# Optimization experiments

Measured on AMD Instinct MI355X. Metric: run time of the kernel, lower is better.

Reference implementation:

```python
import jax, jax.numpy as jnp
import numpy as np

K_HOPS = 3
ALPHA = 0.3
DELTA = 0.5
KL_EPS = 1e-10
BN_EPS = 1e-5
DEG_MIN = 1e-6

B, T, N, F_IN, H, T_OUT = 8, 12, 1536, 1, 64, 12
HID2 = 2 * H  # MLP hidden width = 128


def setup_inputs() -> dict:
    key = jax.random.key(0)
    ks = jax.random.split(key, 20)
    s = 0.05
    TH = T * H
    inp = {
        "x": jax.random.normal(ks[0], (B, T, N, F_IN), jnp.float32),
        # AdaptiveBiDiffConv weights (stored as (in, out))
        "W1": jax.random.normal(ks[1], (F_IN, H), jnp.float32) * s,
        "W2": jax.random.normal(ks[2], (F_IN, H), jnp.float32) * s,
        # encoder MLPBlock: Linear(TH,128) ReLU Linear(128,128) ReLU Linear(128,64) + proj(TH,64), BN(64)
        "enc_w1": jax.random.normal(ks[3], (TH, HID2), jnp.float32) * s,
        "enc_b1": jnp.zeros((HID2,), jnp.float32),
        "enc_w2": jax.random.normal(ks[4], (HID2, HID2), jnp.float32) * s,
        "enc_b2": jnp.zeros((HID2,), jnp.float32),
        "enc_w3": jax.random.normal(ks[5], (HID2, H), jnp.float32) * s,
        "enc_b3": jnp.zeros((H,), jnp.float32),
        "enc_proj": jax.random.normal(ks[6], (TH, H), jnp.float32) * s,
        "enc_bn_g": jnp.ones((H,), jnp.float32),
        "enc_bn_b": jnp.zeros((H,), jnp.float32),
        "enc_bn_m": jnp.zeros((H,), jnp.float32),
        "enc_bn_v": jnp.ones((H,), jnp.float32),
        # decoder MLPBlock: Linear(64,128) ReLU Linear(128,128) ReLU Linear(128,12) + proj(64,12), BN(12)
        "dec_w1": jax.random.normal(ks[7], (H, HID2), jnp.float32) * s,
        "dec_b1": jnp.zeros((HID2,), jnp.float32),
        "dec_w2": jax.random.normal(ks[8], (HID2, HID2), jnp.float32) * s,
        "dec_b2": jnp.zeros((HID2,), jnp.float32),
        "dec_w3": jax.random.normal(ks[9], (HID2, T_OUT), jnp.float32) * s,
        "dec_b3": jnp.zeros((T_OUT,), jnp.float32),
        "dec_proj": jax.random.normal(ks[10], (H, T_OUT), jnp.float32) * s,
        "dec_bn_g": jnp.ones((T_OUT,), jnp.float32),
        "dec_bn_b": jnp.zeros((T_OUT,), jnp.float32),
        "dec_bn_m": jnp.zeros((T_OUT,), jnp.float32),
        "dec_bn_v": jnp.ones((T_OUT,), jnp.float32),
    }
    return inp


def _row_norm(A):
    return A / jnp.maximum(A.sum(-1, keepdims=True), DEG_MIN)


def _mlp_block(z, w1, b1, w2, b2, w3, b3, proj, g, be, m, v):
    h = jax.nn.relu(z @ w1 + b1)
    h = jax.nn.relu(h @ w2 + b2)
    o = (h @ w3 + b3) + z @ proj
    # BatchNorm1d, eval mode over last (channel) axis
    return (o - m) / jnp.sqrt(v + BN_EPS) * g + be


def _forward(x, W1, W2,
             enc_w1, enc_b1, enc_w2, enc_b2, enc_w3, enc_b3, enc_proj,
             enc_bn_g, enc_bn_b, enc_bn_m, enc_bn_v,
             dec_w1, dec_b1, dec_w2, dec_b2, dec_w3, dec_b3, dec_proj,
             dec_bn_g, dec_bn_b, dec_bn_m, dec_bn_v):
    b, t, n, _ = x.shape
    # ---- KL adjacency (fused form: avoids (B,N,N,T) broadcast) ----
    p = jax.nn.softmax(jnp.transpose(x[..., 0], (0, 2, 1)), axis=-1)  # (B,N,T)
    logp = jnp.log(p + KL_EPS)
    # kl[b,i,j] = sum_t p_i (logp_i - logp_j)
    kl = jnp.sum(p * logp, axis=-1, keepdims=True) - jnp.einsum('bit,bjt->bij', p, logp)
    A = (kl < DELTA).astype(x.dtype)  # (B,N,N)
    A_fwd = _row_norm(A)
    A_bwd = _row_norm(jnp.swapaxes(A, -1, -2))
    # ---- bidirectional diffusion conv (x_k never updated in original loop) ----
    x_flow = x[..., :1]                    # (B,T,N,1)
    x_res = x_flow @ W1                    # (B,T,N,H)
    xw = x_flow @ W2                       # (B,T,N,H)
    fwd = jnp.einsum('bij,btjh->btih', A_fwd, xw)
    bwd = jnp.einsum('bij,btjh->btih', A_bwd, xw)
    x_p = jax.nn.relu(x_res + K_HOPS * (ALPHA * fwd + (1.0 - ALPHA) * bwd))
    # ---- temporal MLP encoder/decoder ----
    x_flat = jnp.transpose(x_p, (0, 2, 1, 3)).reshape(b, n, t * x_p.shape[-1])  # (B,N,T*H)
    x_e = _mlp_block(x_flat, enc_w1, enc_b1, enc_w2, enc_b2, enc_w3, enc_b3,
                     enc_proj, enc_bn_g, enc_bn_b, enc_bn_m, enc_bn_v)  # (B,N,H)
    x_d = _mlp_block(x_e, dec_w1, dec_b1, dec_w2, dec_b2, dec_w3, dec_b3,
                     dec_proj, dec_bn_g, dec_bn_b, dec_bn_m, dec_bn_v)  # (B,N,T_out)
    return jnp.transpose(x_d, (0, 2, 1))[..., None]  # (B,T_out,N,1)


def reference(x, W1, W2,
              enc_w1, enc_b1, enc_w2, enc_b2, enc_w3, enc_b3, enc_proj,
              enc_bn_g, enc_bn_b, enc_bn_m, enc_bn_v,
              dec_w1, dec_b1, dec_w2, dec_b2, dec_w3, dec_b3, dec_proj,
              dec_bn_g, dec_bn_b, dec_bn_m, dec_bn_v):
    return _forward(x, W1, W2,
                    enc_w1, enc_b1, enc_w2, enc_b2, enc_w3, enc_b3, enc_proj,
                    enc_bn_g, enc_bn_b, enc_bn_m, enc_bn_v,
                    dec_w1, dec_b1, dec_w2, dec_b2, dec_w3, dec_b3, dec_proj,
                    dec_bn_g, dec_bn_b, dec_bn_m, dec_bn_v)
```

## Files before the change

### kernel.cpp

```cpp
#include <hip/hip_runtime.h>
#include <hip/hip_bf16.h>


namespace {

constexpr int Nn = 1536, TOUT = 12;

typedef __attribute__((ext_vector_type(8))) short bf8;
typedef __attribute__((ext_vector_type(4))) float f4;
typedef unsigned short ush;

__device__ __forceinline__ float b2f(__hip_bfloat16 v) { return __bfloat162float(v); }
__device__ __forceinline__ ush f2bu(float f) {
  union { __hip_bfloat16 h; ush u; } c; c.h = __float2bfloat16(f); return c.u;
}
__device__ __forceinline__ float bu2f(ush u) {
  union { unsigned int i; float f; } c; c.i = ((unsigned)u) << 16; return c.f;
}
__device__ __forceinline__ float ldraw(const void* p, size_t i, int fl) {
  return fl ? ((const float*)p)[i] : b2f(((const __hip_bfloat16*)p)[i]);
}

__device__ __forceinline__ int detect_fl(const void* x, int tid) {
  __shared__ int cnt;
  if (tid == 0) cnt = 0;
  __syncthreads();
  const ush* u = (const ush*)x;
  int c = 0;
#pragma unroll
  for (int s = 0; s < 16; ++s) {
    ush v = u[tid + s * 256];
    if (((v >> 7) & 0xFF) >= 140) c++;
  }
  atomicAdd(&cnt, c);
  __syncthreads();
  return (cnt > 64) ? 1 : 0;
}

struct SmallTab { const void* src[16]; int n[16]; int off[16]; };
struct RepTab { const void* src[8]; int Nc[8]; int NCT[8]; int lb[9]; };

__global__ __launch_bounds__(256) void prep_all(
    const void* __restrict__ xraw, SmallTab st, RepTab rt,
    int* __restrict__ flag, float* __restrict__ CS,
    float* __restrict__ xT, float* __restrict__ sd,
    ush* __restrict__ pA, ush* __restrict__ lA,
    ush* __restrict__ phi16, ush* __restrict__ plo16,
    ush* __restrict__ lhi16, ush* __restrict__ llo16,
    ush* __restrict__ Xc, ush* __restrict__ Wf) {
  int tid = threadIdx.x;
  int fl = detect_fl(xraw, tid);
  int blk = blockIdx.x;

  if (blk < 48) {
    int row = blk * 256 + tid;
    int b = row / Nn, n = row - b * Nn;
    float xv[12];
#pragma unroll
    for (int t = 0; t < 12; ++t)
      xv[t] = ldraw(xraw, (size_t)(b * 12 + t) * Nn + n, fl);
    float mx = xv[0];
#pragma unroll
    for (int t = 1; t < 12; ++t) mx = fmaxf(mx, xv[t]);
    float e[12], Z = 0.f;
#pragma unroll
    for (int t = 0; t < 12; ++t) { e[t] = expf(xv[t] - mx); Z += e[t]; }
    float invZ = 1.f / Z;
    float sacc = 0.f;
    ush pa[32], la[32], ph[16], pl[16], lh[16], ll[16];
#pragma unroll
    for (int k = 0; k < 32; ++k) { pa[k] = 0; la[k] = 0; }
#pragma unroll
    for (int k = 0; k < 16; ++k) { ph[k] = 0; pl[k] = 0; lh[k] = 0; ll[k] = 0; }
#pragma unroll
    for (int t = 0; t < 12; ++t) {
      float pv = e[t] * invZ;
      float lv = logf(pv + 1e-10f);
      sacc += pv * lv;
      xT[(size_t)row * 12 + t] = xv[t];
      ush phv = f2bu(pv);  float plv = pv - bu2f(phv);
      ush lhv = f2bu(lv);  float llv = lv - bu2f(lhv);
      pa[t] = phv; pa[16 + t] = f2bu(plv);
      la[t] = lhv; la[16 + t] = f2bu(llv);
      ph[t] = phv; pl[t] = f2bu(plv);
      lh[t] = lhv; ll[t] = f2bu(llv);
      Xc[((size_t)(b * 16 + t)) * Nn + n] = f2bu(xv[t]);
    }
    Xc[((size_t)(b * 16 + 12)) * Nn + n] = 0x3F80;
#pragma unroll
    for (int t = 13; t < 16; ++t) Xc[((size_t)(b * 16 + t)) * Nn + n] = 0;
    sd[row] = sacc;
    {
      uint4* d = (uint4*)(pA + (size_t)row * 32);
      const uint4* s = (const uint4*)pa;
      d[0] = s[0]; d[1] = s[1]; d[2] = s[2]; d[3] = s[3];
      uint4* d2 = (uint4*)(lA + (size_t)row * 32);
      const uint4* s2 = (const uint4*)la;
      d2[0] = s2[0]; d2[1] = s2[1]; d2[2] = s2[2]; d2[3] = s2[3];
      ((uint4*)(phi16 + (size_t)row * 16))[0] = ((const uint4*)ph)[0];
      ((uint4*)(phi16 + (size_t)row * 16))[1] = ((const uint4*)ph)[1];
      ((uint4*)(plo16 + (size_t)row * 16))[0] = ((const uint4*)pl)[0];
      ((uint4*)(plo16 + (size_t)row * 16))[1] = ((const uint4*)pl)[1];
      ((uint4*)(lhi16 + (size_t)row * 16))[0] = ((const uint4*)lh)[0];
      ((uint4*)(lhi16 + (size_t)row * 16))[1] = ((const uint4*)lh)[1];
      ((uint4*)(llo16 + (size_t)row * 16))[0] = ((const uint4*)ll)[0];
      ((uint4*)(llo16 + (size_t)row * 16))[1] = ((const uint4*)ll)[1];
    }
  } else if (blk < 146) {
    int idx = (blk - 48) * 256 + tid;
    if (idx >= rt.lb[8]) return;
    int mi = 0;
#pragma unroll
    for (int i = 1; i < 8; ++i) if (idx >= rt.lb[i]) mi = i;
    int li = idx - rt.lb[mi];
    int NCT = rt.NCT[mi], Nc = rt.Nc[mi];
    int per = NCT * 64;
    int c0 = li / per, rem = li - c0 * per;
    int ct = rem >> 6, l = rem & 63;
    int q = l >> 4, m = l & 15;
    int col = ct * 16 + m;
    ush* d = Wf + (size_t)idx * 8;
#pragma unroll
    for (int j = 0; j < 8; ++j) {
      int k = c0 * 32 + q * 8 + j;
      d[j] = (col < Nc) ? f2bu(ldraw(rt.src[mi], (size_t)k * Nc + col, fl)) : 0;
    }
  } else {
    for (int i = 0; i < 16; ++i)
      for (int e = tid; e < st.n[i]; e += 256)
        CS[st.off[i] + e] = ldraw(st.src[i], e, fl);
    if (tid == 0) flag[0] = fl;
  }
}

__global__ __launch_bounds__(256, 3) void klmlp(
    const float* __restrict__ xT,
    const ush* __restrict__ pA, const ush* __restrict__ lA,
    const ush* __restrict__ phi16, const ush* __restrict__ plo16,
    const ush* __restrict__ lhi16, const ush* __restrict__ llo16,
    const ush* __restrict__ Xc, const float* __restrict__ sd,
    const float* __restrict__ CS, const ush* __restrict__ Wf,
    const int* __restrict__ flag, void* __restrict__ outp) {
  __shared__ float xs[16][12], ccs[16][12];
  __shared__ float sfs[16][16], sbs[16][16];
  __shared__ float ws1[64], ws2[64];
  __shared__ ush hf[2048], hg[2048], xf[1024];
  __shared__ f4 red[4][64], red2[4][64];
  __shared__ union { ush T[2][4][512]; ush zf[12288]; } u;

  int tid = threadIdx.x, w = tid >> 6, l = tid & 63, q = l >> 4, n = l & 15;
  int bi = blockIdx.x;
  int r0 = bi * 16;
  int b = bi / 96;
  int rowb = b * Nn;

  if (tid < 192) {
    int rr = tid / 12, tt = tid - rr * 12;
    xs[rr][tt] = xT[(size_t)(r0 + rr) * 12 + tt];
  }

  {
    bf8 z8 = {0, 0, 0, 0, 0, 0, 0, 0};
    bf8 aP = *(const bf8*)(pA + ((size_t)(r0 + n)) * 32 + q * 8);
    bf8 aL = *(const bf8*)(lA + ((size_t)(r0 + n)) * 32 + q * 8);
    bf8 aPh = (q < 2) ? aP : z8;
    bf8 aLh = (q < 2) ? aL : z8;
    float selfI[4];
#pragma unroll
    for (int r = 0; r < 4; ++r) selfI[r] = sd[r0 + q * 4 + r];

    f4 accF = {0.f, 0.f, 0.f, 0.f}, accB = {0.f, 0.f, 0.f, 0.f};

    for (int jp = 0; jp < 12; ++jp) {
      int jl = w * 384 + jp * 32;
#pragma unroll
      for (int hh = 0; hh < 2; ++hh) {
        int jh = jl + hh * 16;
        size_t bb = ((size_t)(rowb + jh + n)) * 16 + (q & 1) * 8;
        bf8 bLh = *(const bf8*)(lhi16 + bb);
        bf8 bLo = *(const bf8*)(llo16 + bb);
        bf8 bPh = *(const bf8*)(phi16 + bb);
        bf8 bPo = *(const bf8*)(plo16 + bb);
        float selfJ = sd[rowb + jh + n];

        f4 s1 = {0.f, 0.f, 0.f, 0.f}, s2 = {0.f, 0.f, 0.f, 0.f};
        s1 = __builtin_amdgcn_mfma_f32_16x16x32_bf16(aP, bLh, s1, 0, 0, 0);
        s1 = __builtin_amdgcn_mfma_f32_16x16x32_bf16(aPh, bLo, s1, 0, 0, 0);
        s2 = __builtin_amdgcn_mfma_f32_16x16x32_bf16(aL, bPh, s2, 0, 0, 0);
        s2 = __builtin_amdgcn_mfma_f32_16x16x32_bf16(aLh, bPo, s2, 0, 0, 0);

        int qk = n >> 3, kj = n & 7;
#pragma unroll
        for (int r = 0; r < 4; ++r) {
          int pos = hh * 256 + (qk * 16 + q * 4 + r) * 8 + kj;
          u.T[0][w][pos] = (selfI[r] - s1[r] < 0.5f) ? (ush)0x3F80 : (ush)0;
          u.T[1][w][pos] = (selfJ - s2[r] < 0.5f) ? (ush)0x3F80 : (ush)0;
        }
      }
      bf8 af1 = *(const bf8*)(&u.T[0][w][(size_t)l * 8]);
      bf8 af2 = *(const bf8*)(&u.T[1][w][(size_t)l * 8]);
      bf8 xfr = *(const bf8*)(Xc + ((size_t)(b * 16 + n)) * Nn + jl + q * 8);
      accF = __builtin_amdgcn_mfma_f32_16x16x32_bf16(af1, xfr, accF, 0, 0, 0);
      accB = __builtin_amdgcn_mfma_f32_16x16x32_bf16(af2, xfr, accB, 0, 0, 0);
    }
    red[w][l] = accF;
    red2[w][l] = accB;
  }
  __syncthreads();

  if (w == 0) {
    f4 s = red[0][l] + red[1][l] + red[2][l] + red[3][l];
#pragma unroll
    for (int r = 0; r < 4; ++r) sfs[q * 4 + r][n] = s[r];
  } else if (w == 1) {
    f4 s = red2[0][l] + red2[1][l] + red2[2][l] + red2[3][l];
#pragma unroll
    for (int r = 0; r < 4; ++r) sbs[q * 4 + r][n] = s[r];
  } else if (w == 2) {
    ws1[l] = CS[l];
  } else {
    ws2[l] = CS[64 + l];
  }
  __syncthreads();
  if (tid < 192) {
    int rr = tid / 12, tt = tid - rr * 12;
    float irs = 1.f / fmaxf(sfs[rr][12], 1e-6f);
    float ics = 1.f / fmaxf(sbs[rr][12], 1e-6f);
    ccs[rr][tt] = 3.0f * (0.3f * sfs[rr][tt] * irs + 0.7f * sbs[rr][tt] * ics);
  }
  __syncthreads();

  auto zregen = [&](int c0) -> bf8 {
    int t = c0 >> 1, h0 = (c0 & 1) * 32 + q * 8;
    float xv = xs[n][t], cv = ccs[n][t];
    union { bf8 v; ush uu[8]; } au;
#pragma unroll
    for (int j = 0; j < 8; ++j)
      au.uu[j] = f2bu(fmaxf(fmaf(xv, ws1[h0 + j], cv * ws2[h0 + j]), 0.f));
    return au.v;
  };
  auto fpos = [&](int ct, int r) -> int {
    return ((ct >> 1) * 64 + ((ct & 1) * 2 + (n >> 3)) * 16 + q * 4 + r) * 8 + (n & 7);
  };

#pragma unroll
  for (int u6 = 0; u6 < 6; ++u6) {
    int c0 = w * 6 + u6;
    bf8 v = zregen(c0);
    *(bf8*)(&u.zf[((size_t)c0 * 64 + l) * 8]) = v;
  }
  __syncthreads();

  {
    f4 a0 = {0.f, 0.f, 0.f, 0.f}, a1 = {0.f, 0.f, 0.f, 0.f};
    for (int c0 = 0; c0 < 24; ++c0) {
      bf8 a = *(const bf8*)(&u.zf[((size_t)c0 * 64 + l) * 8]);
      const ush* wb = Wf + ((size_t)(c0 * 8 + 2 * w) * 64 + l) * 8;
      bf8 b0 = *(const bf8*)wb;
      bf8 b1 = *(const bf8*)(wb + 512);
      a0 = __builtin_amdgcn_mfma_f32_16x16x32_bf16(a, b0, a0, 0, 0, 0);
      a1 = __builtin_amdgcn_mfma_f32_16x16x32_bf16(a, b1, a1, 0, 0, 0);
    }
#pragma unroll
    for (int u2 = 0; u2 < 2; ++u2) {
      int ct = 2 * w + u2;
      f4 acc = u2 ? a1 : a0;
      float bz = CS[128 + ct * 16 + n];
#pragma unroll
      for (int r = 0; r < 4; ++r)
        hf[fpos(ct, r)] = f2bu(fmaxf(acc[r] + bz, 0.f));
    }
  }
  __syncthreads();

  {
    f4 a0 = {0.f, 0.f, 0.f, 0.f}, a1 = {0.f, 0.f, 0.f, 0.f};
    for (int c0 = 0; c0 < 4; ++c0) {
      bf8 a = *(const bf8*)(&hf[(size_t)(c0 * 64 + l) * 8]);
      const ush* wb = Wf + 98304 + ((size_t)(c0 * 8 + 2 * w) * 64 + l) * 8;
      bf8 b0 = *(const bf8*)wb;
      bf8 b1 = *(const bf8*)(wb + 512);
      a0 = __builtin_amdgcn_mfma_f32_16x16x32_bf16(a, b0, a0, 0, 0, 0);
      a1 = __builtin_amdgcn_mfma_f32_16x16x32_bf16(a, b1, a1, 0, 0, 0);
    }
    __syncthreads();
#pragma unroll
    for (int u2 = 0; u2 < 2; ++u2) {
      int ct = 2 * w + u2;
      f4 acc = u2 ? a1 : a0;
      float bz = CS[256 + ct * 16 + n];
#pragma unroll
      for (int r = 0; r < 4; ++r)
        hg[fpos(ct, r)] = f2bu(fmaxf(acc[r] + bz, 0.f));
    }
  }
  __syncthreads();

  {
    f4 a3 = {0.f, 0.f, 0.f, 0.f};
    for (int c0 = 0; c0 < 4; ++c0) {
      bf8 a = *(const bf8*)(&hg[(size_t)(c0 * 64 + l) * 8]);
      bf8 bb = *(const bf8*)(Wf + 114688 + ((size_t)(c0 * 4 + w) * 64 + l) * 8);
      a3 = __builtin_amdgcn_mfma_f32_16x16x32_bf16(a, bb, a3, 0, 0, 0);
    }
    for (int c0 = 0; c0 < 24; ++c0) {
      bf8 a = *(const bf8*)(&u.zf[((size_t)c0 * 64 + l) * 8]);
      bf8 bb = *(const bf8*)(Wf + 122880 + ((size_t)(c0 * 4 + w) * 64 + l) * 8);
      a3 = __builtin_amdgcn_mfma_f32_16x16x32_bf16(a, bb, a3, 0, 0, 0);
    }
    int col = w * 16 + n;
    float g = CS[448 + col], be = CS[512 + col], mm = CS[576 + col], vv = CS[640 + col];
    float sc = g / sqrtf(vv + 1e-5f);
    float sh = be - mm * sc;
    float bz = CS[384 + col];
#pragma unroll
    for (int r = 0; r < 4; ++r)
      xf[fpos(w, r)] = f2bu((a3[r] + bz) * sc + sh);
  }
  __syncthreads();

  {
    f4 a0 = {0.f, 0.f, 0.f, 0.f}, a1 = {0.f, 0.f, 0.f, 0.f};
    for (int c0 = 0; c0 < 2; ++c0) {
      bf8 a = *(const bf8*)(&xf[(size_t)(c0 * 64 + l) * 8]);
      const ush* wb = Wf + 172032 + ((size_t)(c0 * 8 + 2 * w) * 64 + l) * 8;
      bf8 b0 = *(const bf8*)wb;
      bf8 b1 = *(const bf8*)(wb + 512);
      a0 = __builtin_amdgcn_mfma_f32_16x16x32_bf16(a, b0, a0, 0, 0, 0);
      a1 = __builtin_amdgcn_mfma_f32_16x16x32_bf16(a, b1, a1, 0, 0, 0);
    }
    __syncthreads();
#pragma unroll
    for (int u2 = 0; u2 < 2; ++u2) {
      int ct = 2 * w + u2;
      f4 acc = u2 ? a1 : a0;
      float bz = CS[704 + ct * 16 + n];
#pragma unroll
      for (int r = 0; r < 4; ++r)
        hf[fpos(ct, r)] = f2bu(fmaxf(acc[r] + bz, 0.f));
    }
  }
  __syncthreads();

  {
    f4 a0 = {0.f, 0.f, 0.f, 0.f}, a1 = {0.f, 0.f, 0.f, 0.f};
    for (int c0 = 0; c0 < 4; ++c0) {
      bf8 a = *(const bf8*)(&hf[(size_t)(c0 * 64 + l) * 8]);
      const ush* wb = Wf + 180224 + ((size_t)(c0 * 8 + 2 * w) * 64 + l) * 8;
      bf8 b0 = *(const bf8*)wb;
      bf8 b1 = *(const bf8*)(wb + 512);
      a0 = __builtin_amdgcn_mfma_f32_16x16x32_bf16(a, b0, a0, 0, 0, 0);
      a1 = __builtin_amdgcn_mfma_f32_16x16x32_bf16(a, b1, a1, 0, 0, 0);
    }
    __syncthreads();
#pragma unroll
    for (int u2 = 0; u2 < 2; ++u2) {
      int ct = 2 * w + u2;
      f4 acc = u2 ? a1 : a0;
      float bz = CS[832 + ct * 16 + n];
#pragma unroll
      for (int r = 0; r < 4; ++r)
        hg[fpos(ct, r)] = f2bu(fmaxf(acc[r] + bz, 0.f));
    }
  }
  __syncthreads();

  {
    f4 ao = {0.f, 0.f, 0.f, 0.f};
    {
      bf8 a = *(const bf8*)(&hg[(size_t)(w * 64 + l) * 8]);
      bf8 bb = *(const bf8*)(Wf + 196608 + ((size_t)w * 64 + l) * 8);
      ao = __builtin_amdgcn_mfma_f32_16x16x32_bf16(a, bb, ao, 0, 0, 0);
    }
    if (w < 2) {
      bf8 a = *(const bf8*)(&xf[(size_t)(w * 64 + l) * 8]);
      bf8 bb = *(const bf8*)(Wf + 198656 + ((size_t)w * 64 + l) * 8);
      ao = __builtin_amdgcn_mfma_f32_16x16x32_bf16(a, bb, ao, 0, 0, 0);
    }
    red[w][l] = ao;
  }
  __syncthreads();
  if (w == 0) {
    f4 s = red[0][l] + red[1][l] + red[2][l] + red[3][l];
    int fl = flag[0];
    if (n < 12) {
      float bz = CS[960 + n];
      float g = CS[972 + n], be = CS[984 + n], mm = CS[996 + n], vv = CS[1008 + n];
      float sc = g / sqrtf(vv + 1e-5f);
      float sh = be - mm * sc;
#pragma unroll
      for (int r = 0; r < 4; ++r) {
        int row = r0 + q * 4 + r;
        int bb2 = row / Nn, nn2 = row - bb2 * Nn;
        size_t oi = ((size_t)bb2 * TOUT + n) * Nn + nn2;
        float ov = (s[r] + bz) * sc + sh;
        if (fl) ((float*)outp)[oi] = ov;
        else    ((ush*)outp)[oi] = f2bu(ov);
      }
    }
  }
}

}

extern "C" void kernel_launch(void* const* d_in, const int* in_sizes, int n_in,
                              void* d_out, int out_size, void* d_ws, size_t ws_size,
                              hipStream_t stream) {
  float* f = (float*)d_ws;
  int* flag = (int*)d_ws;
  float* CS  = f + 16;
  float* xT  = f + 1040;
  float* sd  = f + 148496;
  ush* U = (ush*)(f + 160784);
  ush* pA    = U;
  ush* lA    = U + 393216;
  ush* phi16 = U + 786432;
  ush* plo16 = U + 983040;
  ush* lhi16 = U + 1179648;
  ush* llo16 = U + 1376256;
  ush* Xc    = U + 1572864;
  ush* Wf    = U + 1769472;

  SmallTab st;
  {
    const int idxs[16] = {1, 2, 4, 6, 8, 10, 11, 12, 13, 15, 17, 19, 21, 22, 23, 24};
    const int ns[16]   = {64, 64, 128, 128, 64, 64, 64, 64, 64, 128, 128, 12, 12, 12, 12, 12};
    int off = 0;
    for (int i = 0; i < 16; ++i) {
      st.src[i] = d_in[idxs[i]]; st.n[i] = ns[i]; st.off[i] = off; off += ns[i];
    }
  }
  RepTab rt;
  {
    const int idxs[8]  = {3, 5, 7, 9, 14, 16, 18, 20};
    const int rNc[8]   = {128, 128, 64, 64, 128, 128, 12, 12};
    const int rNCT[8]  = {8, 8, 4, 4, 8, 8, 1, 1};
    const int rlb[9]   = {0, 12288, 14336, 15360, 21504, 22528, 24576, 24832, 24960};
    for (int i = 0; i < 8; ++i) {
      rt.src[i] = d_in[idxs[i]]; rt.Nc[i] = rNc[i]; rt.NCT[i] = rNCT[i];
    }
    for (int i = 0; i < 9; ++i) rt.lb[i] = rlb[i];
  }

  prep_all<<<147, 256, 0, stream>>>(d_in[0], st, rt, flag, CS, xT, sd,
                                    pA, lA, phi16, plo16, lhi16, llo16, Xc, Wf);
  klmlp<<<768, 256, 0, stream>>>(xT, pA, lA, phi16, plo16, lhi16, llo16,
                                 Xc, sd, CS, Wf, flag, d_out);
}
```

Before: 142.4 us.

## Drop redundant pA/lA/xT buffers and split prep rows across four threads

The prep kernel no longer writes the duplicated pA/lA packed arrays or the transposed xT copy. The main kernel now rebuilds its A fragments from the phi/plo/lhi/llo arrays and reads x directly from the raw input. Prep work is spread over four threads per row (192 blocks instead of 48), with a shared-memory reduction for the self-entropy term. This cuts global write traffic and adds parallelism in prep, at the cost of scalar ush stores in place of vector stores and an extra barrier.

```diff
diff --git a/kernel.cpp b/kernel.cpp
--- a/kernel.cpp
+++ b/kernel.cpp
@@ -43,22 +43,23 @@
 __global__ __launch_bounds__(256) void prep_all(
     const void* __restrict__ xraw, SmallTab st, RepTab rt,
     int* __restrict__ flag, float* __restrict__ CS,
-    float* __restrict__ xT, float* __restrict__ sd,
-    ush* __restrict__ pA, ush* __restrict__ lA,
+    float* __restrict__ sd,
     ush* __restrict__ phi16, ush* __restrict__ plo16,
     ush* __restrict__ lhi16, ush* __restrict__ llo16,
     ush* __restrict__ Xc, ush* __restrict__ Wf) {
+  __shared__ float lvs[64][12];
   int tid = threadIdx.x;
   int fl = detect_fl(xraw, tid);
   int blk = blockIdx.x;
 
-  if (blk < 48) {
-    int row = blk * 256 + tid;
-    int b = row / Nn, n = row - b * Nn;
+  if (blk < 192) {
+    int rl = tid >> 2, sub = tid & 3;
+    int row = blk * 64 + rl;
+    int b = row / Nn, nn = row - b * Nn;
     float xv[12];
 #pragma unroll
     for (int t = 0; t < 12; ++t)
-      xv[t] = ldraw(xraw, (size_t)(b * 12 + t) * Nn + n, fl);
+      xv[t] = ldraw(xraw, (size_t)(b * 12 + t) * Nn + nn, fl);
     float mx = xv[0];
 #pragma unroll
     for (int t = 1; t < 12; ++t) mx = fmaxf(mx, xv[t]);
@@ -66,48 +67,38 @@
 #pragma unroll
     for (int t = 0; t < 12; ++t) { e[t] = expf(xv[t] - mx); Z += e[t]; }
     float invZ = 1.f / Z;
-    float sacc = 0.f;
-    ush pa[32], la[32], ph[16], pl[16], lh[16], ll[16];
-#pragma unroll
-    for (int k = 0; k < 32; ++k) { pa[k] = 0; la[k] = 0; }
-#pragma unroll
-    for (int k = 0; k < 16; ++k) { ph[k] = 0; pl[k] = 0; lh[k] = 0; ll[k] = 0; }
-#pragma unroll
-    for (int t = 0; t < 12; ++t) {
+#pragma unroll
+    for (int u = 0; u < 3; ++u) {
+      int t = sub * 3 + u;
       float pv = e[t] * invZ;
       float lv = logf(pv + 1e-10f);
-      sacc += pv * lv;
-      xT[(size_t)row * 12 + t] = xv[t];
+      lvs[rl][t] = lv;
       ush phv = f2bu(pv);  float plv = pv - bu2f(phv);
       ush lhv = f2bu(lv);  float llv = lv - bu2f(lhv);
-      pa[t] = phv; pa[16 + t] = f2bu(plv);
-      la[t] = lhv; la[16 + t] = f2bu(llv);
-      ph[t] = phv; pl[t] = f2bu(plv);
-      lh[t] = lhv; ll[t] = f2bu(llv);
-      Xc[((size_t)(b * 16 + t)) * Nn + n] = f2bu(xv[t]);
-    }
-    Xc[((size_t)(b * 16 + 12)) * Nn + n] = 0x3F80;
-#pragma unroll
-    for (int t = 13; t < 16; ++t) Xc[((size_t)(b * 16 + t)) * Nn + n] = 0;
-    sd[row] = sacc;
+      phi16[(size_t)row * 16 + t] = phv;
+      plo16[(size_t)row * 16 + t] = f2bu(plv);
+      lhi16[(size_t)row * 16 + t] = lhv;
+      llo16[(size_t)row * 16 + t] = f2bu(llv);
+      Xc[((size_t)(b * 16 + t)) * Nn + nn] = f2bu(xv[t]);
+    }
     {
-      uint4* d = (uint4*)(pA + (size_t)row * 32);
-      const uint4* s = (const uint4*)pa;
-      d[0] = s[0]; d[1] = s[1]; d[2] = s[2]; d[3] = s[3];
-      uint4* d2 = (uint4*)(lA + (size_t)row * 32);
-      const uint4* s2 = (const uint4*)la;
-      d2[0] = s2[0]; d2[1] = s2[1]; d2[2] = s2[2]; d2[3] = s2[3];
-      ((uint4*)(phi16 + (size_t)row * 16))[0] = ((const uint4*)ph)[0];
-      ((uint4*)(phi16 + (size_t)row * 16))[1] = ((const uint4*)ph)[1];
-      ((uint4*)(plo16 + (size_t)row * 16))[0] = ((const uint4*)pl)[0];
-      ((uint4*)(plo16 + (size_t)row * 16))[1] = ((const uint4*)pl)[1];
-      ((uint4*)(lhi16 + (size_t)row * 16))[0] = ((const uint4*)lh)[0];
-      ((uint4*)(lhi16 + (size_t)row * 16))[1] = ((const uint4*)lh)[1];
-      ((uint4*)(llo16 + (size_t)row * 16))[0] = ((const uint4*)ll)[0];
-      ((uint4*)(llo16 + (size_t)row * 16))[1] = ((const uint4*)ll)[1];
-    }
-  } else if (blk < 146) {
-    int idx = (blk - 48) * 256 + tid;
+      int t = 12 + sub;
+      phi16[(size_t)row * 16 + t] = 0;
+      plo16[(size_t)row * 16 + t] = 0;
+      lhi16[(size_t)row * 16 + t] = 0;
+      llo16[(size_t)row * 16 + t] = 0;
+      Xc[((size_t)(b * 16 + t)) * Nn + nn] = (sub == 0) ? (ush)0x3F80 : (ush)0;
+    }
+    __syncthreads();
+    if (sub == 0) {
+      float sacc = 0.f;
+#pragma unroll
+      for (int t = 0; t < 12; ++t)
+        sacc = fmaf(e[t] * invZ, lvs[rl][t], sacc);
+      sd[row] = sacc;
+    }
+  } else if (blk < 290) {
+    int idx = (blk - 192) * 256 + tid;
     if (idx >= rt.lb[8]) return;
     int mi = 0;
 #pragma unroll
@@ -134,8 +125,7 @@
 }
 
 __global__ __launch_bounds__(256, 3) void klmlp(
-    const float* __restrict__ xT,
-    const ush* __restrict__ pA, const ush* __restrict__ lA,
+    const void* __restrict__ xraw,
     const ush* __restrict__ phi16, const ush* __restrict__ plo16,
     const ush* __restrict__ lhi16, const ush* __restrict__ llo16,
     const ush* __restrict__ Xc, const float* __restrict__ sd,
@@ -153,16 +143,21 @@
   int r0 = bi * 16;
   int b = bi / 96;
   int rowb = b * Nn;
+  int fl = flag[0];
 
   if (tid < 192) {
     int rr = tid / 12, tt = tid - rr * 12;
-    xs[rr][tt] = xT[(size_t)(r0 + rr) * 12 + tt];
+    xs[rr][tt] = ldraw(xraw, (size_t)(b * 12 + tt) * Nn + (r0 - rowb + rr), fl);
   }
 
   {
     bf8 z8 = {0, 0, 0, 0, 0, 0, 0, 0};
-    bf8 aP = *(const bf8*)(pA + ((size_t)(r0 + n)) * 32 + q * 8);
-    bf8 aL = *(const bf8*)(lA + ((size_t)(r0 + n)) * 32 + q * 8);
+    bf8 aP = (q < 2)
+        ? *(const bf8*)(phi16 + ((size_t)(r0 + n)) * 16 + q * 8)
+        : *(const bf8*)(plo16 + ((size_t)(r0 + n)) * 16 + (q - 2) * 8);
+    bf8 aL = (q < 2)
+        ? *(const bf8*)(lhi16 + ((size_t)(r0 + n)) * 16 + q * 8)
+        : *(const bf8*)(llo16 + ((size_t)(r0 + n)) * 16 + (q - 2) * 8);
     bf8 aPh = (q < 2) ? aP : z8;
     bf8 aLh = (q < 2) ? aL : z8;
     float selfI[4];
@@ -382,7 +377,6 @@
   __syncthreads();
   if (w == 0) {
     f4 s = red[0][l] + red[1][l] + red[2][l] + red[3][l];
-    int fl = flag[0];
     if (n < 12) {
       float bz = CS[960 + n];
       float g = CS[972 + n], be = CS[984 + n], mm = CS[996 + n], vv = CS[1008 + n];
@@ -409,17 +403,14 @@
   float* f = (float*)d_ws;
   int* flag = (int*)d_ws;
   float* CS  = f + 16;
-  float* xT  = f + 1040;
-  float* sd  = f + 148496;
-  ush* U = (ush*)(f + 160784);
-  ush* pA    = U;
-  ush* lA    = U + 393216;
-  ush* phi16 = U + 786432;
-  ush* plo16 = U + 983040;
-  ush* lhi16 = U + 1179648;
-  ush* llo16 = U + 1376256;
-  ush* Xc    = U + 1572864;
-  ush* Wf    = U + 1769472;
+  float* sd  = f + 1040;
+  ush* U = (ush*)(f + 13328);
+  ush* phi16 = U;
+  ush* plo16 = U + 196608;
+  ush* lhi16 = U + 393216;
+  ush* llo16 = U + 589824;
+  ush* Xc    = U + 786432;
+  ush* Wf    = U + 983040;
 
   SmallTab st;
   {
@@ -442,8 +433,8 @@
     for (int i = 0; i < 9; ++i) rt.lb[i] = rlb[i];
   }
 
-  prep_all<<<147, 256, 0, stream>>>(d_in[0], st, rt, flag, CS, xT, sd,
-                                    pA, lA, phi16, plo16, lhi16, llo16, Xc, Wf);
-  klmlp<<<768, 256, 0, stream>>>(xT, pA, lA, phi16, plo16, lhi16, llo16,
+  prep_all<<<291, 256, 0, stream>>>(d_in[0], st, rt, flag, CS, sd,
+                                    phi16, plo16, lhi16, llo16, Xc, Wf);
+  klmlp<<<768, 256, 0, stream>>>(d_in[0], phi16, plo16, lhi16, llo16,
                                  Xc, sd, CS, Wf, flag, d_out);
 }
```

Measured after the change: 140.6 us (median of 2 runs). No clear change (-1.3%).
